# Optimization experiments

Measured on AMD Instinct MI355X. Metric: run time of the kernel, lower is better.

The kernel has to match this reference:

```python
import jax, jax.numpy as jnp
import numpy as np

D = 1024  # input_dim


def setup_inputs() -> dict:
    key = jax.random.key(0)
    ks = jax.random.split(key, 7)
    scale = 1.0 / np.sqrt(D)
    x = jax.random.normal(ks[0], (4, D, 2048), dtype=jnp.float32)
    Wq = jax.random.uniform(ks[1], (D, D), jnp.float32, -scale, scale)
    bq = jax.random.uniform(ks[2], (D,), jnp.float32, -scale, scale)
    Wk = jax.random.uniform(ks[3], (D, D), jnp.float32, -scale, scale)
    bk = jax.random.uniform(ks[4], (D,), jnp.float32, -scale, scale)
    Wv = jax.random.uniform(ks[5], (D, D), jnp.float32, -scale, scale)
    bv = jax.random.uniform(ks[6], (D,), jnp.float32, -scale, scale)
    return {"x": x, "Wq": Wq, "bq": bq, "Wk": Wk, "bk": bk, "Wv": Wv, "bv": bv}


def reference(x, Wq, bq, Wk, bk, Wv, bv):
    # x: [B, D, S] -> [B, S, D]
    xt = jnp.transpose(x, (0, 2, 1))
    # torch nn.Linear: y = x @ W^T + b
    q = jnp.einsum('bsd,ed->bse', xt, Wq) + bq
    k = jnp.einsum('bsd,ed->bse', xt, Wk) + bk
    v = jnp.einsum('bsd,ed->bse', xt, Wv) + bv
    scores = jnp.einsum('bse,bte->bst', q, k) / jnp.sqrt(jnp.float32(D))
    attn = jax.nn.softmax(scores, axis=2)
    out = jnp.einsum('bst,bte->bse', attn, v)  # [B, S, D]
    return out
```

## Files before the change

### kernel.cpp

```cpp
#include <hip/hip_runtime.h>
#include <stdint.h>

typedef unsigned short us16;
typedef unsigned short us8  __attribute__((ext_vector_type(8)));
typedef unsigned short us4v __attribute__((ext_vector_type(4)));
typedef __bf16         bf16x8 __attribute__((ext_vector_type(8)));
typedef float          f32x4  __attribute__((ext_vector_type(4)));

__device__ __forceinline__ us16 f2bf(float f) {
    union { float f; unsigned int u; } c; c.f = f;
    unsigned int u = (c.u + 0x7fffu + ((c.u >> 16) & 1u)) >> 16;
    return (us16)u;
}

__device__ __forceinline__ void async16(const us16* g, us16* l) {
    __builtin_amdgcn_global_load_lds(
        (const __attribute__((address_space(1))) unsigned int*)g,
        (__attribute__((address_space(3))) unsigned int*)l,
        16, 0, 0);
}

template <int EPI, int MI>
__device__ __forceinline__ void gemm_core(
        const us16* __restrict__ A, const us16* __restrict__ B,
        void* __restrict__ C, const float* __restrict__ bias,
        float* __restrict__ L,
        int M, int K, int x, int y, us16* lds) {
    constexpr int BM     = MI * 32;
    constexpr int BOFF   = BM * 64;
    constexpr int BUF    = (BM + 256) * 64;
    constexpr int ACALLS = BM / 64;
    constexpr int PMI    = MI / 4;

    const int tid  = threadIdx.x;
    const int lane = tid & 63, wid = tid >> 6;
    const int l15  = lane & 15, quad = lane >> 4;
    const int wm   = wid >> 2, wn = wid & 3;
    const int m0   = x * BM, n0 = y * 256;

    const int srow = tid >> 3;
    const int sc   = ((tid & 7) ^ (srow & 7)) * 8;
    const us16* Ag = A + (size_t)(m0 + srow) * K + sc;
    const us16* Bg = B + (size_t)(n0 + srow) * K + sc;
    const int sl   = tid * 8;

    f32x4 acc[MI][4] = {};
    const int NT = K >> 6;

#pragma unroll
    for (int c = 0; c < ACALLS; c++) async16(Ag + (size_t)(c * 64) * K, lds + c * 4096 + sl);
#pragma unroll
    for (int c = 0; c < 4; c++)      async16(Bg + (size_t)(c * 64) * K, lds + BOFF + c * 4096 + sl);

    for (int t = 0; t < NT; t++) {
        const us16* cur = lds + (t & 1) * BUF;
        __syncthreads();

        if (t + 1 < NT) {
            us16* nxt = lds + ((t + 1) & 1) * BUF;
            const size_t ko = (size_t)(t + 1) * 64;
#pragma unroll
            for (int c = 0; c < ACALLS; c++) async16(Ag + (size_t)(c * 64) * K + ko, nxt + c * 4096 + sl);
#pragma unroll
            for (int c = 0; c < 4; c++)      async16(Bg + (size_t)(c * 64) * K + ko, nxt + BOFF + c * 4096 + sl);
        }

        bf16x8 bf[4][2];
#pragma unroll
        for (int nj = 0; nj < 4; nj++) {
            const int rb = wn * 64 + nj * 16 + l15;
#pragma unroll
            for (int ks = 0; ks < 2; ks++)
                bf[nj][ks] = *(const bf16x8*)(cur + BOFF + rb * 64 + ((ks * 4 + quad) ^ (rb & 7)) * 8);
        }
        bf16x8 af[2][PMI][2];
#pragma unroll
        for (int i = 0; i < PMI; i++) {
            const int ra = wm * (MI * 16) + i * 16 + l15;
#pragma unroll
            for (int ks = 0; ks < 2; ks++)
                af[0][i][ks] = *(const bf16x8*)(cur + ra * 64 + ((ks * 4 + quad) ^ (ra & 7)) * 8);
        }

#pragma unroll
        for (int p = 0; p < 4; p++) {
            if (p < 3) {
#pragma unroll
                for (int i = 0; i < PMI; i++) {
                    const int ra = wm * (MI * 16) + ((p + 1) * PMI + i) * 16 + l15;
#pragma unroll
                    for (int ks = 0; ks < 2; ks++)
                        af[(p + 1) & 1][i][ks] = *(const bf16x8*)(cur + ra * 64 + ((ks * 4 + quad) ^ (ra & 7)) * 8);
                }
            }
            __builtin_amdgcn_s_setprio(1);
#pragma unroll
            for (int ks = 0; ks < 2; ks++)
#pragma unroll
                for (int i = 0; i < PMI; i++)
#pragma unroll
                    for (int nj = 0; nj < 4; nj++)
                        acc[p * PMI + i][nj] = __builtin_amdgcn_mfma_f32_16x16x32_bf16(
                            af[p & 1][i][ks], bf[nj][ks], acc[p * PMI + i][nj], 0, 0, 0);
            __builtin_amdgcn_s_setprio(0);
        }
    }

    if (EPI == 2) {
        const float scale = 0.03125f;
        float rs[4] = {0.f, 0.f, 0.f, 0.f};
#pragma unroll
        for (int i = 0; i < MI; i++) {
            const int mb = m0 + wm * (MI * 16) + i * 16 + quad * 4;
#pragma unroll
            for (int j = 0; j < 4; j++) {
                const int n = n0 + wn * 64 + j * 16 + l15;
                f32x4 v = acc[i][j];
                const float e0 = __expf(v[0] * scale), e1 = __expf(v[1] * scale);
                const float e2 = __expf(v[2] * scale), e3 = __expf(v[3] * scale);
                rs[j] += (e0 + e1) + (e2 + e3);
                us4v st = { f2bf(e0), f2bf(e1), f2bf(e2), f2bf(e3) };
                *(us4v*)((us16*)C + (size_t)n * M + mb) = st;
            }
        }
#pragma unroll
        for (int j = 0; j < 4; j++) {
            rs[j] += __shfl_xor(rs[j], 16, 64);
            rs[j] += __shfl_xor(rs[j], 32, 64);
        }
        if (quad == 0) {
#pragma unroll
            for (int j = 0; j < 4; j++)
                atomicAdd(&L[n0 + wn * 64 + j * 16 + l15], rs[j]);
        }
        return;
    }

#pragma unroll
    for (int i = 0; i < MI; i++) {
        const int mb = m0 + wm * (MI * 16) + i * 16 + quad * 4;
        float b0 = 0.f, b1 = 0.f, b2 = 0.f, b3 = 0.f;
        if (EPI == 0) {
            float4 bv4 = *(const float4*)(bias + mb);
            b0 = bv4.x; b1 = bv4.y; b2 = bv4.z; b3 = bv4.w;
        }
#pragma unroll
        for (int j = 0; j < 4; j++) {
            const int n = n0 + wn * 64 + j * 16 + l15;
            f32x4 v = acc[i][j];
            if (EPI == 3) {
                const float inv = 1.0f / L[n];
                float4 st;
                st.x = v[0] * inv; st.y = v[1] * inv;
                st.z = v[2] * inv; st.w = v[3] * inv;
                *(float4*)((float*)C + (size_t)n * M + mb) = st;
            } else {
                const float bn = (EPI == 1) ? bias[n] : 0.0f;
                us4v st = { f2bf(v[0] + b0 + bn), f2bf(v[1] + b1 + bn),
                            f2bf(v[2] + b2 + bn), f2bf(v[3] + b3 + bn) };
                *(us4v*)((us16*)C + (size_t)n * M + mb) = st;
            }
        }
    }
}

__device__ __forceinline__ void strip_xy(int lin, int gy, int& x, int& y) {
    const int within = lin & (4 * gy - 1);
    x = (lin / (4 * gy)) * 4 + (within & 3);
    y = within >> 2;
}

__global__ __launch_bounds__(256)
void prep(const float* __restrict__ x, us16* __restrict__ xt,
          const float* __restrict__ wq, const float* __restrict__ wk,
          const float* __restrict__ wv, us16* __restrict__ wb) {
    __shared__ us16 tile[64 * 65];
    const int id = blockIdx.x;
    const int t = threadIdx.x;
    if (id < 2048) {
        const int s0 = (id & 31) * 64, d0 = ((id >> 5) & 15) * 64, b = id >> 9;
        const float* xp = x + ((size_t)b * 1024 + d0) * 2048 + s0;
        const int r = t >> 4, c4 = t & 15;
#pragma unroll
        for (int i = 0; i < 4; i++) {
            float4 v = *(const float4*)(xp + (size_t)(r + 16 * i) * 2048 + c4 * 4);
            const int d = r + 16 * i;
            tile[(c4 * 4 + 0) * 65 + d] = f2bf(v.x);
            tile[(c4 * 4 + 1) * 65 + d] = f2bf(v.y);
            tile[(c4 * 4 + 2) * 65 + d] = f2bf(v.z);
            tile[(c4 * 4 + 3) * 65 + d] = f2bf(v.w);
        }
        __syncthreads();
        us16* op = xt + ((size_t)b * 2048 + s0) * 1024 + d0;
#pragma unroll
        for (int i = 0; i < 2; i++) {
            const int u = t + 256 * i;
            const int s = u >> 3, c8 = u & 7;
            us8 o;
#pragma unroll
            for (int j = 0; j < 8; j++) o[j] = tile[s * 65 + c8 * 8 + j];
            *(us8*)(op + (size_t)s * 1024 + c8 * 8) = o;
        }
    } else {
        const int cid = id - 2048;
        const int mb = cid >> 10;
        const float* src = (mb == 0) ? wq : (mb == 1) ? wk : wv;
        const size_t off = ((size_t)(cid & 1023) * 256 + t) * 4;
        float4 v = *(const float4*)(src + off);
        us4v o = { f2bf(v.x), f2bf(v.y), f2bf(v.z), f2bf(v.w) };
        *(us4v*)(wb + (size_t)mb * 1048576 + off) = o;
    }
}

__global__ __launch_bounds__(512)
void qkv(const us16* __restrict__ Wb, const us16* __restrict__ XT,
         us16* __restrict__ Qb, us16* __restrict__ Kb, us16* __restrict__ VT,
         const float* __restrict__ bq, const float* __restrict__ bk,
         const float* __restrict__ bv) {
    __shared__ __align__(16) us16 lds[65536];
    const int id = blockIdx.x;
    const long long sXT = 2097152;
    if (id < 256) {
        const int z = id >> 5, zz = z & 3;
        const bool isK = z >= 4;
        int x, y; strip_xy(id & 31, 8, x, y);
        const us16* A = Wb + (isK ? 1048576 : 0);
        const us16* B = XT + (size_t)zz * sXT;
        us16* C = (isK ? Kb : Qb) + (size_t)zz * sXT;
        gemm_core<0, 8>(A, B, (void*)C, isK ? bk : bq, nullptr, 1024, 1024, x, y, lds);
    } else {
        const int id2 = id - 256;
        const int z = id2 >> 6;
        int x, y; strip_xy(id2 & 63, 4, x, y);
        gemm_core<1, 4>(XT + (size_t)z * sXT, Wb + 2097152,
                        (void*)(VT + (size_t)z * sXT), bv, nullptr,
                        2048, 1024, x, y, lds);
    }
}

__global__ __launch_bounds__(512)
void scores_k(const us16* __restrict__ Kb, const us16* __restrict__ Qb,
              us16* __restrict__ Sb, float* __restrict__ L) {
    __shared__ __align__(16) us16 lds[65536];
    const long long sXT = 2097152, sSS = 4194304;
    const int z = blockIdx.z;
    int x, y; strip_xy(blockIdx.x + 8 * blockIdx.y, 8, x, y);
    gemm_core<2, 8>(Kb + (size_t)z * sXT, Qb + (size_t)z * sXT,
                    (void*)(Sb + (size_t)z * sSS), nullptr, L + z * 2048,
                    2048, 1024, x, y, lds);
}

__global__ __launch_bounds__(512)
void out_k(const us16* __restrict__ VT, const us16* __restrict__ Sb,
           float* __restrict__ L, float* __restrict__ out) {
    __shared__ __align__(16) us16 lds[49152];
    const long long sXT = 2097152, sSS = 4194304;
    const int z = blockIdx.z;
    int x, y; strip_xy(blockIdx.x + 8 * blockIdx.y, 8, x, y);
    gemm_core<3, 4>(VT + (size_t)z * sXT, Sb + (size_t)z * sSS,
                    (void*)(out + (size_t)z * sXT), nullptr, L + z * 2048,
                    1024, 2048, x, y, lds);
}

extern "C" void kernel_launch(void* const* d_in, const int* in_sizes, int n_in,
                              void* d_out, int out_size, void* d_ws, size_t ws_size,
                              hipStream_t stream) {
    const float* x  = (const float*)d_in[0];
    const float* Wq = (const float*)d_in[1];
    const float* bq = (const float*)d_in[2];
    const float* Wk = (const float*)d_in[3];
    const float* bk = (const float*)d_in[4];
    const float* Wv = (const float*)d_in[5];
    const float* bv = (const float*)d_in[6];
    float* out = (float*)d_out;
    char* ws = (char*)d_ws;

    const size_t SZ = 16777216;
    us16* Qb = (us16*)(ws);
    us16* Kb = (us16*)(ws + SZ);
    us16* VT = (us16*)(ws + 2 * SZ);
    us16* XT = (us16*)(ws + 3 * SZ);
    us16* Wb = (us16*)(ws + 4 * SZ);
    us16* Sb = (us16*)(ws + 3 * SZ);
    float* Lb = (float*)(ws + 5 * SZ);

    hipMemsetAsync(Lb, 0, 4 * 2048 * sizeof(float), stream);
    prep<<<dim3(5120, 1, 1), dim3(256, 1, 1), 0, stream>>>(x, XT, Wq, Wk, Wv, Wb);
    qkv<<<dim3(512, 1, 1), dim3(512, 1, 1), 0, stream>>>(Wb, XT, Qb, Kb, VT, bq, bk, bv);
    scores_k<<<dim3(8, 8, 4), dim3(512, 1, 1), 0, stream>>>(Kb, Qb, Sb, Lb);
    out_k<<<dim3(8, 8, 4), dim3(512, 1, 1), 0, stream>>>(VT, Sb, Lb, out);
}
```

Measured before the change: 222.7 us.

## Software-pipeline LDS fragment loads across k-tiles with split last-phase MFMAs

The GEMM main loop is restructured so the first B and A fragments of the next k-tile are read from LDS while the last phase's MFMAs of the current tile are still issuing. The final phase is split into two halves of the N columns, with the B fragment reloads interleaved between them after a vmcnt wait and barrier. The aim is to hide LDS read latency at the tile boundary so the MFMA pipe is not left idle. In exchange there is an extra barrier per iteration, higher register pressure, and a more fragile ordering between the async global-to-LDS loads and the reads that follow them.

```diff
diff --git a/kernel.cpp b/kernel.cpp
--- a/kernel.cpp
+++ b/kernel.cpp
@@ -51,47 +51,46 @@
     for (int c = 0; c < ACALLS; c++) async16(Ag + (size_t)(c * 64) * K, lds + c * 4096 + sl);
 #pragma unroll
     for (int c = 0; c < 4; c++)      async16(Bg + (size_t)(c * 64) * K, lds + BOFF + c * 4096 + sl);
+    __syncthreads();
+
+    bf16x8 bf[4][2];
+    bf16x8 af[2][PMI][2];
+#pragma unroll
+    for (int nj = 0; nj < 4; nj++) {
+        const int rb = wn * 64 + nj * 16 + l15;
+#pragma unroll
+        for (int ks = 0; ks < 2; ks++)
+            bf[nj][ks] = *(const bf16x8*)(lds + BOFF + rb * 64 + ((ks * 4 + quad) ^ (rb & 7)) * 8);
+    }
+#pragma unroll
+    for (int i = 0; i < PMI; i++) {
+        const int ra = wm * (MI * 16) + i * 16 + l15;
+#pragma unroll
+        for (int ks = 0; ks < 2; ks++)
+            af[0][i][ks] = *(const bf16x8*)(lds + ra * 64 + ((ks * 4 + quad) ^ (ra & 7)) * 8);
+    }
 
     for (int t = 0; t < NT; t++) {
         const us16* cur = lds + (t & 1) * BUF;
-        __syncthreads();
+        const us16* nxt = lds + ((t + 1) & 1) * BUF;
 
         if (t + 1 < NT) {
-            us16* nxt = lds + ((t + 1) & 1) * BUF;
+            us16* nb = lds + ((t + 1) & 1) * BUF;
             const size_t ko = (size_t)(t + 1) * 64;
 #pragma unroll
-            for (int c = 0; c < ACALLS; c++) async16(Ag + (size_t)(c * 64) * K + ko, nxt + c * 4096 + sl);
-#pragma unroll
-            for (int c = 0; c < 4; c++)      async16(Bg + (size_t)(c * 64) * K + ko, nxt + BOFF + c * 4096 + sl);
-        }
-
-        bf16x8 bf[4][2];
-#pragma unroll
-        for (int nj = 0; nj < 4; nj++) {
-            const int rb = wn * 64 + nj * 16 + l15;
-#pragma unroll
-            for (int ks = 0; ks < 2; ks++)
-                bf[nj][ks] = *(const bf16x8*)(cur + BOFF + rb * 64 + ((ks * 4 + quad) ^ (rb & 7)) * 8);
-        }
-        bf16x8 af[2][PMI][2];
-#pragma unroll
-        for (int i = 0; i < PMI; i++) {
-            const int ra = wm * (MI * 16) + i * 16 + l15;
-#pragma unroll
-            for (int ks = 0; ks < 2; ks++)
-                af[0][i][ks] = *(const bf16x8*)(cur + ra * 64 + ((ks * 4 + quad) ^ (ra & 7)) * 8);
-        }
-
-#pragma unroll
-        for (int p = 0; p < 4; p++) {
-            if (p < 3) {
-#pragma unroll
-                for (int i = 0; i < PMI; i++) {
-                    const int ra = wm * (MI * 16) + ((p + 1) * PMI + i) * 16 + l15;
-#pragma unroll
-                    for (int ks = 0; ks < 2; ks++)
-                        af[(p + 1) & 1][i][ks] = *(const bf16x8*)(cur + ra * 64 + ((ks * 4 + quad) ^ (ra & 7)) * 8);
-                }
+            for (int c = 0; c < ACALLS; c++) async16(Ag + (size_t)(c * 64) * K + ko, nb + c * 4096 + sl);
+#pragma unroll
+            for (int c = 0; c < 4; c++)      async16(Bg + (size_t)(c * 64) * K + ko, nb + BOFF + c * 4096 + sl);
+        }
+
+#pragma unroll
+        for (int p = 0; p < 3; p++) {
+#pragma unroll
+            for (int i = 0; i < PMI; i++) {
+                const int ra = wm * (MI * 16) + ((p + 1) * PMI + i) * 16 + l15;
+#pragma unroll
+                for (int ks = 0; ks < 2; ks++)
+                    af[(p + 1) & 1][i][ks] = *(const bf16x8*)(cur + ra * 64 + ((ks * 4 + quad) ^ (ra & 7)) * 8);
             }
             __builtin_amdgcn_s_setprio(1);
 #pragma unroll
@@ -104,6 +103,65 @@
                             af[p & 1][i][ks], bf[nj][ks], acc[p * PMI + i][nj], 0, 0, 0);
             __builtin_amdgcn_s_setprio(0);
         }
+
+        if (t + 1 < NT) {
+            asm volatile("s_waitcnt vmcnt(0)" ::: "memory");
+            __builtin_amdgcn_s_barrier();
+            __builtin_amdgcn_sched_barrier(0);
+            __builtin_amdgcn_s_setprio(1);
+#pragma unroll
+            for (int ks = 0; ks < 2; ks++)
+#pragma unroll
+                for (int i = 0; i < PMI; i++)
+#pragma unroll
+                    for (int nj = 0; nj < 2; nj++)
+                        acc[3 * PMI + i][nj] = __builtin_amdgcn_mfma_f32_16x16x32_bf16(
+                            af[1][i][ks], bf[nj][ks], acc[3 * PMI + i][nj], 0, 0, 0);
+            __builtin_amdgcn_s_setprio(0);
+#pragma unroll
+            for (int nj = 0; nj < 2; nj++) {
+                const int rb = wn * 64 + nj * 16 + l15;
+#pragma unroll
+                for (int ks = 0; ks < 2; ks++)
+                    bf[nj][ks] = *(const bf16x8*)(nxt + BOFF + rb * 64 + ((ks * 4 + quad) ^ (rb & 7)) * 8);
+            }
+            __builtin_amdgcn_s_setprio(1);
+#pragma unroll
+            for (int ks = 0; ks < 2; ks++)
+#pragma unroll
+                for (int i = 0; i < PMI; i++)
+#pragma unroll
+                    for (int nj = 2; nj < 4; nj++)
+                        acc[3 * PMI + i][nj] = __builtin_amdgcn_mfma_f32_16x16x32_bf16(
+                            af[1][i][ks], bf[nj][ks], acc[3 * PMI + i][nj], 0, 0, 0);
+            __builtin_amdgcn_s_setprio(0);
+#pragma unroll
+            for (int nj = 2; nj < 4; nj++) {
+                const int rb = wn * 64 + nj * 16 + l15;
+#pragma unroll
+                for (int ks = 0; ks < 2; ks++)
+                    bf[nj][ks] = *(const bf16x8*)(nxt + BOFF + rb * 64 + ((ks * 4 + quad) ^ (rb & 7)) * 8);
+            }
+#pragma unroll
+            for (int i = 0; i < PMI; i++) {
+                const int ra = wm * (MI * 16) + i * 16 + l15;
+#pragma unroll
+                for (int ks = 0; ks < 2; ks++)
+                    af[0][i][ks] = *(const bf16x8*)(nxt + ra * 64 + ((ks * 4 + quad) ^ (ra & 7)) * 8);
+            }
+        } else {
+            __builtin_amdgcn_s_setprio(1);
+#pragma unroll
+            for (int ks = 0; ks < 2; ks++)
+#pragma unroll
+                for (int i = 0; i < PMI; i++)
+#pragma unroll
+                    for (int nj = 0; nj < 4; nj++)
+                        acc[3 * PMI + i][nj] = __builtin_amdgcn_mfma_f32_16x16x32_bf16(
+                            af[1][i][ks], bf[nj][ks], acc[3 * PMI + i][nj], 0, 0, 0);
+            __builtin_amdgcn_s_setprio(0);
+        }
+        __syncthreads();
     }
 
     if (EPI == 2) {
```

Measured after the change: 236.4 us. +6.2%, slower.

## Switch GEMM core to 32x32x16 MFMA tiles and fold L-buffer memset into prep

Applied to the files above, without the earlier changes.

The shared GEMM core now uses 32x32x16 bf16 MFMA instructions with 16-wide accumulators in place of 16x16x32 ones, and the LDS fragment loads and all epilogues (bias, exp/row-sum, normalize) are remapped to the 32x32 output layout. Block tile sizes stay the same. The larger MFMA shape cuts the LDS fragment reads per FLOP and the instruction count. Separately, the hipMemsetAsync that zeroed the softmax denominator buffer is replaced by four extra blocks in the prep kernel, removing one launch. The new epilogue indexing changes store patterns and must match the 32x32 accumulator layout to stay correct.

```diff
diff --git a/kernel.cpp b/kernel.cpp
--- a/kernel.cpp
+++ b/kernel.cpp
@@ -5,7 +5,7 @@
 typedef unsigned short us8  __attribute__((ext_vector_type(8)));
 typedef unsigned short us4v __attribute__((ext_vector_type(4)));
 typedef __bf16         bf16x8 __attribute__((ext_vector_type(8)));
-typedef float          f32x4  __attribute__((ext_vector_type(4)));
+typedef float          f32x16 __attribute__((ext_vector_type(16)));
 
 __device__ __forceinline__ us16 f2bf(float f) {
     union { float f; unsigned int u; } c; c.f = f;
@@ -20,21 +20,20 @@
         16, 0, 0);
 }
 
-template <int EPI, int MI>
+template <int EPI, int MF>
 __device__ __forceinline__ void gemm_core(
         const us16* __restrict__ A, const us16* __restrict__ B,
         void* __restrict__ C, const float* __restrict__ bias,
         float* __restrict__ L,
         int M, int K, int x, int y, us16* lds) {
-    constexpr int BM     = MI * 32;
+    constexpr int BM     = MF * 64;
     constexpr int BOFF   = BM * 64;
     constexpr int BUF    = (BM + 256) * 64;
-    constexpr int ACALLS = BM / 64;
-    constexpr int PMI    = MI / 4;
+    constexpr int ACALLS = MF;
 
     const int tid  = threadIdx.x;
     const int lane = tid & 63, wid = tid >> 6;
-    const int l15  = lane & 15, quad = lane >> 4;
+    const int l31  = lane & 31, half = lane >> 5;
     const int wm   = wid >> 2, wn = wid & 3;
     const int m0   = x * BM, n0 = y * 256;
 
@@ -44,7 +43,7 @@
     const us16* Bg = B + (size_t)(n0 + srow) * K + sc;
     const int sl   = tid * 8;
 
-    f32x4 acc[MI][4] = {};
+    f32x16 acc[MF][2] = {};
     const int NT = K >> 6;
 
 #pragma unroll
@@ -65,100 +64,102 @@
             for (int c = 0; c < 4; c++)      async16(Bg + (size_t)(c * 64) * K + ko, nxt + BOFF + c * 4096 + sl);
         }
 
-        bf16x8 bf[4][2];
-#pragma unroll
-        for (int nj = 0; nj < 4; nj++) {
-            const int rb = wn * 64 + nj * 16 + l15;
-#pragma unroll
-            for (int ks = 0; ks < 2; ks++)
-                bf[nj][ks] = *(const bf16x8*)(cur + BOFF + rb * 64 + ((ks * 4 + quad) ^ (rb & 7)) * 8);
-        }
-        bf16x8 af[2][PMI][2];
-#pragma unroll
-        for (int i = 0; i < PMI; i++) {
-            const int ra = wm * (MI * 16) + i * 16 + l15;
-#pragma unroll
-            for (int ks = 0; ks < 2; ks++)
-                af[0][i][ks] = *(const bf16x8*)(cur + ra * 64 + ((ks * 4 + quad) ^ (ra & 7)) * 8);
-        }
-
-#pragma unroll
-        for (int p = 0; p < 4; p++) {
-            if (p < 3) {
-#pragma unroll
-                for (int i = 0; i < PMI; i++) {
-                    const int ra = wm * (MI * 16) + ((p + 1) * PMI + i) * 16 + l15;
-#pragma unroll
-                    for (int ks = 0; ks < 2; ks++)
-                        af[(p + 1) & 1][i][ks] = *(const bf16x8*)(cur + ra * 64 + ((ks * 4 + quad) ^ (ra & 7)) * 8);
+        bf16x8 bf[2][4];
+#pragma unroll
+        for (int nf = 0; nf < 2; nf++) {
+            const int rb = wn * 64 + nf * 32 + l31;
+#pragma unroll
+            for (int ks = 0; ks < 4; ks++)
+                bf[nf][ks] = *(const bf16x8*)(cur + BOFF + rb * 64 + ((ks * 2 + half) ^ (rb & 7)) * 8);
+        }
+        bf16x8 af[2][4];
+        {
+            const int ra = wm * (MF * 32) + l31;
+#pragma unroll
+            for (int ks = 0; ks < 4; ks++)
+                af[0][ks] = *(const bf16x8*)(cur + ra * 64 + ((ks * 2 + half) ^ (ra & 7)) * 8);
+        }
+
+#pragma unroll
+        for (int p = 0; p < MF; p++) {
+            if (p + 1 < MF) {
+                const int ra = wm * (MF * 32) + (p + 1) * 32 + l31;
+#pragma unroll
+                for (int ks = 0; ks < 4; ks++)
+                    af[(p + 1) & 1][ks] = *(const bf16x8*)(cur + ra * 64 + ((ks * 2 + half) ^ (ra & 7)) * 8);
+            }
+            __builtin_amdgcn_s_setprio(1);
+#pragma unroll
+            for (int ks = 0; ks < 4; ks++)
+#pragma unroll
+                for (int nf = 0; nf < 2; nf++)
+                    acc[p][nf] = __builtin_amdgcn_mfma_f32_32x32x16_bf16(
+                        af[p & 1][ks], bf[nf][ks], acc[p][nf], 0, 0, 0);
+            __builtin_amdgcn_s_setprio(0);
+        }
+    }
+
+    if (EPI == 2) {
+        const float scale = 0.03125f;
+        float rs[2] = {0.f, 0.f};
+#pragma unroll
+        for (int mf = 0; mf < MF; mf++) {
+#pragma unroll
+            for (int nf = 0; nf < 2; nf++) {
+                const int n = n0 + wn * 64 + nf * 32 + l31;
+                const int mbase = m0 + wm * (MF * 32) + mf * 32 + 4 * half;
+                f32x16 v = acc[mf][nf];
+#pragma unroll
+                for (int g = 0; g < 4; g++) {
+                    const float e0 = __expf(v[4 * g + 0] * scale);
+                    const float e1 = __expf(v[4 * g + 1] * scale);
+                    const float e2 = __expf(v[4 * g + 2] * scale);
+                    const float e3 = __expf(v[4 * g + 3] * scale);
+                    rs[nf] += (e0 + e1) + (e2 + e3);
+                    us4v st = { f2bf(e0), f2bf(e1), f2bf(e2), f2bf(e3) };
+                    *(us4v*)((us16*)C + (size_t)n * M + mbase + 8 * g) = st;
                 }
             }
-            __builtin_amdgcn_s_setprio(1);
-#pragma unroll
-            for (int ks = 0; ks < 2; ks++)
-#pragma unroll
-                for (int i = 0; i < PMI; i++)
-#pragma unroll
-                    for (int nj = 0; nj < 4; nj++)
-                        acc[p * PMI + i][nj] = __builtin_amdgcn_mfma_f32_16x16x32_bf16(
-                            af[p & 1][i][ks], bf[nj][ks], acc[p * PMI + i][nj], 0, 0, 0);
-            __builtin_amdgcn_s_setprio(0);
-        }
-    }
-
-    if (EPI == 2) {
-        const float scale = 0.03125f;
-        float rs[4] = {0.f, 0.f, 0.f, 0.f};
-#pragma unroll
-        for (int i = 0; i < MI; i++) {
-            const int mb = m0 + wm * (MI * 16) + i * 16 + quad * 4;
-#pragma unroll
-            for (int j = 0; j < 4; j++) {
-                const int n = n0 + wn * 64 + j * 16 + l15;
-                f32x4 v = acc[i][j];
-                const float e0 = __expf(v[0] * scale), e1 = __expf(v[1] * scale);
-                const float e2 = __expf(v[2] * scale), e3 = __expf(v[3] * scale);
-                rs[j] += (e0 + e1) + (e2 + e3);
-                us4v st = { f2bf(e0), f2bf(e1), f2bf(e2), f2bf(e3) };
-                *(us4v*)((us16*)C + (size_t)n * M + mb) = st;
-            }
-        }
-#pragma unroll
-        for (int j = 0; j < 4; j++) {
-            rs[j] += __shfl_xor(rs[j], 16, 64);
-            rs[j] += __shfl_xor(rs[j], 32, 64);
-        }
-        if (quad == 0) {
-#pragma unroll
-            for (int j = 0; j < 4; j++)
-                atomicAdd(&L[n0 + wn * 64 + j * 16 + l15], rs[j]);
+        }
+#pragma unroll
+        for (int nf = 0; nf < 2; nf++) rs[nf] += __shfl_xor(rs[nf], 32, 64);
+        if (half == 0) {
+#pragma unroll
+            for (int nf = 0; nf < 2; nf++)
+                atomicAdd(&L[n0 + wn * 64 + nf * 32 + l31], rs[nf]);
         }
         return;
     }
 
 #pragma unroll
-    for (int i = 0; i < MI; i++) {
-        const int mb = m0 + wm * (MI * 16) + i * 16 + quad * 4;
-        float b0 = 0.f, b1 = 0.f, b2 = 0.f, b3 = 0.f;
-        if (EPI == 0) {
-            float4 bv4 = *(const float4*)(bias + mb);
-            b0 = bv4.x; b1 = bv4.y; b2 = bv4.z; b3 = bv4.w;
-        }
-#pragma unroll
-        for (int j = 0; j < 4; j++) {
-            const int n = n0 + wn * 64 + j * 16 + l15;
-            f32x4 v = acc[i][j];
+    for (int mf = 0; mf < MF; mf++) {
+#pragma unroll
+        for (int nf = 0; nf < 2; nf++) {
+            const int n = n0 + wn * 64 + nf * 32 + l31;
+            const int mbase = m0 + wm * (MF * 32) + mf * 32 + 4 * half;
+            f32x16 v = acc[mf][nf];
             if (EPI == 3) {
                 const float inv = 1.0f / L[n];
-                float4 st;
-                st.x = v[0] * inv; st.y = v[1] * inv;
-                st.z = v[2] * inv; st.w = v[3] * inv;
-                *(float4*)((float*)C + (size_t)n * M + mb) = st;
+#pragma unroll
+                for (int g = 0; g < 4; g++) {
+                    float4 st;
+                    st.x = v[4 * g + 0] * inv; st.y = v[4 * g + 1] * inv;
+                    st.z = v[4 * g + 2] * inv; st.w = v[4 * g + 3] * inv;
+                    *(float4*)((float*)C + (size_t)n * M + mbase + 8 * g) = st;
+                }
             } else {
                 const float bn = (EPI == 1) ? bias[n] : 0.0f;
-                us4v st = { f2bf(v[0] + b0 + bn), f2bf(v[1] + b1 + bn),
-                            f2bf(v[2] + b2 + bn), f2bf(v[3] + b3 + bn) };
-                *(us4v*)((us16*)C + (size_t)n * M + mb) = st;
+#pragma unroll
+                for (int g = 0; g < 4; g++) {
+                    float b0 = bn, b1 = bn, b2 = bn, b3 = bn;
+                    if (EPI == 0) {
+                        float4 bv4 = *(const float4*)(bias + mbase + 8 * g);
+                        b0 = bv4.x; b1 = bv4.y; b2 = bv4.z; b3 = bv4.w;
+                    }
+                    us4v st = { f2bf(v[4 * g + 0] + b0), f2bf(v[4 * g + 1] + b1),
+                                f2bf(v[4 * g + 2] + b2), f2bf(v[4 * g + 3] + b3) };
+                    *(us4v*)((us16*)C + (size_t)n * M + mbase + 8 * g) = st;
+                }
             }
         }
     }
@@ -173,7 +174,8 @@
 __global__ __launch_bounds__(256)
 void prep(const float* __restrict__ x, us16* __restrict__ xt,
           const float* __restrict__ wq, const float* __restrict__ wk,
-          const float* __restrict__ wv, us16* __restrict__ wb) {
+          const float* __restrict__ wv, us16* __restrict__ wb,
+          float* __restrict__ Lb) {
     __shared__ us16 tile[64 * 65];
     const int id = blockIdx.x;
     const int t = threadIdx.x;
@@ -201,7 +203,7 @@
             for (int j = 0; j < 8; j++) o[j] = tile[s * 65 + c8 * 8 + j];
             *(us8*)(op + (size_t)s * 1024 + c8 * 8) = o;
         }
-    } else {
+    } else if (id < 5120) {
         const int cid = id - 2048;
         const int mb = cid >> 10;
         const float* src = (mb == 0) ? wq : (mb == 1) ? wk : wv;
@@ -209,6 +211,11 @@
         float4 v = *(const float4*)(src + off);
         us4v o = { f2bf(v.x), f2bf(v.y), f2bf(v.z), f2bf(v.w) };
         *(us4v*)(wb + (size_t)mb * 1048576 + off) = o;
+    } else {
+        float4 z = { 0.f, 0.f, 0.f, 0.f };
+        float* p = Lb + (size_t)(id - 5120) * 2048 + t * 8;
+        *(float4*)(p) = z;
+        *(float4*)(p + 4) = z;
     }
 }
 
@@ -227,12 +234,12 @@
         const us16* A = Wb + (isK ? 1048576 : 0);
         const us16* B = XT + (size_t)zz * sXT;
         us16* C = (isK ? Kb : Qb) + (size_t)zz * sXT;
-        gemm_core<0, 8>(A, B, (void*)C, isK ? bk : bq, nullptr, 1024, 1024, x, y, lds);
+        gemm_core<0, 4>(A, B, (void*)C, isK ? bk : bq, nullptr, 1024, 1024, x, y, lds);
     } else {
         const int id2 = id - 256;
         const int z = id2 >> 6;
         int x, y; strip_xy(id2 & 63, 4, x, y);
-        gemm_core<1, 4>(XT + (size_t)z * sXT, Wb + 2097152,
+        gemm_core<1, 2>(XT + (size_t)z * sXT, Wb + 2097152,
                         (void*)(VT + (size_t)z * sXT), bv, nullptr,
                         2048, 1024, x, y, lds);
     }
@@ -245,7 +252,7 @@
     const long long sXT = 2097152, sSS = 4194304;
     const int z = blockIdx.z;
     int x, y; strip_xy(blockIdx.x + 8 * blockIdx.y, 8, x, y);
-    gemm_core<2, 8>(Kb + (size_t)z * sXT, Qb + (size_t)z * sXT,
+    gemm_core<2, 4>(Kb + (size_t)z * sXT, Qb + (size_t)z * sXT,
                     (void*)(Sb + (size_t)z * sSS), nullptr, L + z * 2048,
                     2048, 1024, x, y, lds);
 }
@@ -257,7 +264,7 @@
     const long long sXT = 2097152, sSS = 4194304;
     const int z = blockIdx.z;
     int x, y; strip_xy(blockIdx.x + 8 * blockIdx.y, 8, x, y);
-    gemm_core<3, 4>(VT + (size_t)z * sXT, Sb + (size_t)z * sSS,
+    gemm_core<3, 2>(VT + (size_t)z * sXT, Sb + (size_t)z * sSS,
                     (void*)(out + (size_t)z * sXT), nullptr, L + z * 2048,
                     1024, 2048, x, y, lds);
 }
@@ -284,8 +291,7 @@
     us16* Sb = (us16*)(ws + 3 * SZ);
     float* Lb = (float*)(ws + 5 * SZ);
 
-    hipMemsetAsync(Lb, 0, 4 * 2048 * sizeof(float), stream);
-    prep<<<dim3(5120, 1, 1), dim3(256, 1, 1), 0, stream>>>(x, XT, Wq, Wk, Wv, Wb);
+    prep<<<dim3(5124, 1, 1), dim3(256, 1, 1), 0, stream>>>(x, XT, Wq, Wk, Wv, Wb, Lb);
     qkv<<<dim3(512, 1, 1), dim3(512, 1, 1), 0, stream>>>(Wb, XT, Qb, Kb, VT, bq, bk, bv);
     scores_k<<<dim3(8, 8, 4), dim3(512, 1, 1), 0, stream>>>(Kb, Qb, Sb, Lb);
     out_k<<<dim3(8, 8, 4), dim3(512, 1, 1), 0, stream>>>(VT, Sb, Lb, out);
```

Measured after the change: 233.1 us. 4.7% more time.

## Single-buffer LDS in QKV GEMM and fold L zeroing into prep

Applied to the files above, without the earlier changes.

Adds a single-buffered mode to the shared GEMM core and uses it for the QKV projection kernel, halving its LDS allocation so more workgroups can be resident per CU. In that mode each K-step loads, synchronizes and then computes, giving up the overlap of global loads with MFMA work in exchange for occupancy. Separately, the memset of the softmax normalizer buffer is removed and done by four extra blocks in the prep kernel, saving one launch.

```diff
diff --git a/kernel.cpp b/kernel.cpp
--- a/kernel.cpp
+++ b/kernel.cpp
@@ -20,7 +20,7 @@
         16, 0, 0);
 }
 
-template <int EPI, int MI>
+template <int EPI, int MI, bool SB>
 __device__ __forceinline__ void gemm_core(
         const us16* __restrict__ A, const us16* __restrict__ B,
         void* __restrict__ C, const float* __restrict__ bias,
@@ -47,22 +47,35 @@
     f32x4 acc[MI][4] = {};
     const int NT = K >> 6;
 
-#pragma unroll
-    for (int c = 0; c < ACALLS; c++) async16(Ag + (size_t)(c * 64) * K, lds + c * 4096 + sl);
-#pragma unroll
-    for (int c = 0; c < 4; c++)      async16(Bg + (size_t)(c * 64) * K, lds + BOFF + c * 4096 + sl);
+    if (!SB) {
+#pragma unroll
+        for (int c = 0; c < ACALLS; c++) async16(Ag + (size_t)(c * 64) * K, lds + c * 4096 + sl);
+#pragma unroll
+        for (int c = 0; c < 4; c++)      async16(Bg + (size_t)(c * 64) * K, lds + BOFF + c * 4096 + sl);
+    }
 
     for (int t = 0; t < NT; t++) {
-        const us16* cur = lds + (t & 1) * BUF;
-        __syncthreads();
-
-        if (t + 1 < NT) {
-            us16* nxt = lds + ((t + 1) & 1) * BUF;
-            const size_t ko = (size_t)(t + 1) * 64;
-#pragma unroll
-            for (int c = 0; c < ACALLS; c++) async16(Ag + (size_t)(c * 64) * K + ko, nxt + c * 4096 + sl);
-#pragma unroll
-            for (int c = 0; c < 4; c++)      async16(Bg + (size_t)(c * 64) * K + ko, nxt + BOFF + c * 4096 + sl);
+        const us16* cur;
+        if (SB) {
+            if (t) __syncthreads();
+            const size_t ko = (size_t)t * 64;
+#pragma unroll
+            for (int c = 0; c < ACALLS; c++) async16(Ag + (size_t)(c * 64) * K + ko, lds + c * 4096 + sl);
+#pragma unroll
+            for (int c = 0; c < 4; c++)      async16(Bg + (size_t)(c * 64) * K + ko, lds + BOFF + c * 4096 + sl);
+            __syncthreads();
+            cur = lds;
+        } else {
+            cur = lds + (t & 1) * BUF;
+            __syncthreads();
+            if (t + 1 < NT) {
+                us16* nxt = lds + ((t + 1) & 1) * BUF;
+                const size_t ko = (size_t)(t + 1) * 64;
+#pragma unroll
+                for (int c = 0; c < ACALLS; c++) async16(Ag + (size_t)(c * 64) * K + ko, nxt + c * 4096 + sl);
+#pragma unroll
+                for (int c = 0; c < 4; c++)      async16(Bg + (size_t)(c * 64) * K + ko, nxt + BOFF + c * 4096 + sl);
+            }
         }
 
         bf16x8 bf[4][2];
@@ -173,7 +186,8 @@
 __global__ __launch_bounds__(256)
 void prep(const float* __restrict__ x, us16* __restrict__ xt,
           const float* __restrict__ wq, const float* __restrict__ wk,
-          const float* __restrict__ wv, us16* __restrict__ wb) {
+          const float* __restrict__ wv, us16* __restrict__ wb,
+          float* __restrict__ Lb) {
     __shared__ us16 tile[64 * 65];
     const int id = blockIdx.x;
     const int t = threadIdx.x;
@@ -201,7 +215,7 @@
             for (int j = 0; j < 8; j++) o[j] = tile[s * 65 + c8 * 8 + j];
             *(us8*)(op + (size_t)s * 1024 + c8 * 8) = o;
         }
-    } else {
+    } else if (id < 5120) {
         const int cid = id - 2048;
         const int mb = cid >> 10;
         const float* src = (mb == 0) ? wq : (mb == 1) ? wk : wv;
@@ -209,6 +223,11 @@
         float4 v = *(const float4*)(src + off);
         us4v o = { f2bf(v.x), f2bf(v.y), f2bf(v.z), f2bf(v.w) };
         *(us4v*)(wb + (size_t)mb * 1048576 + off) = o;
+    } else {
+        float4 z = { 0.f, 0.f, 0.f, 0.f };
+        float* p = Lb + (size_t)(id - 5120) * 2048 + t * 8;
+        *(float4*)(p) = z;
+        *(float4*)(p + 4) = z;
     }
 }
 
@@ -217,7 +236,7 @@
          us16* __restrict__ Qb, us16* __restrict__ Kb, us16* __restrict__ VT,
          const float* __restrict__ bq, const float* __restrict__ bk,
          const float* __restrict__ bv) {
-    __shared__ __align__(16) us16 lds[65536];
+    __shared__ __align__(16) us16 lds[32768];
     const int id = blockIdx.x;
     const long long sXT = 2097152;
     if (id < 256) {
@@ -227,14 +246,14 @@
         const us16* A = Wb + (isK ? 1048576 : 0);
         const us16* B = XT + (size_t)zz * sXT;
         us16* C = (isK ? Kb : Qb) + (size_t)zz * sXT;
-        gemm_core<0, 8>(A, B, (void*)C, isK ? bk : bq, nullptr, 1024, 1024, x, y, lds);
+        gemm_core<0, 8, true>(A, B, (void*)C, isK ? bk : bq, nullptr, 1024, 1024, x, y, lds);
     } else {
         const int id2 = id - 256;
         const int z = id2 >> 6;
         int x, y; strip_xy(id2 & 63, 4, x, y);
-        gemm_core<1, 4>(XT + (size_t)z * sXT, Wb + 2097152,
-                        (void*)(VT + (size_t)z * sXT), bv, nullptr,
-                        2048, 1024, x, y, lds);
+        gemm_core<1, 4, true>(XT + (size_t)z * sXT, Wb + 2097152,
+                              (void*)(VT + (size_t)z * sXT), bv, nullptr,
+                              2048, 1024, x, y, lds);
     }
 }
 
@@ -245,9 +264,9 @@
     const long long sXT = 2097152, sSS = 4194304;
     const int z = blockIdx.z;
     int x, y; strip_xy(blockIdx.x + 8 * blockIdx.y, 8, x, y);
-    gemm_core<2, 8>(Kb + (size_t)z * sXT, Qb + (size_t)z * sXT,
-                    (void*)(Sb + (size_t)z * sSS), nullptr, L + z * 2048,
-                    2048, 1024, x, y, lds);
+    gemm_core<2, 8, false>(Kb + (size_t)z * sXT, Qb + (size_t)z * sXT,
+                           (void*)(Sb + (size_t)z * sSS), nullptr, L + z * 2048,
+                           2048, 1024, x, y, lds);
 }
 
 __global__ __launch_bounds__(512)
@@ -257,9 +276,9 @@
     const long long sXT = 2097152, sSS = 4194304;
     const int z = blockIdx.z;
     int x, y; strip_xy(blockIdx.x + 8 * blockIdx.y, 8, x, y);
-    gemm_core<3, 4>(VT + (size_t)z * sXT, Sb + (size_t)z * sSS,
-                    (void*)(out + (size_t)z * sXT), nullptr, L + z * 2048,
-                    1024, 2048, x, y, lds);
+    gemm_core<3, 4, false>(VT + (size_t)z * sXT, Sb + (size_t)z * sSS,
+                           (void*)(out + (size_t)z * sXT), nullptr, L + z * 2048,
+                           1024, 2048, x, y, lds);
 }
 
 extern "C" void kernel_launch(void* const* d_in, const int* in_sizes, int n_in,
@@ -284,8 +303,7 @@
     us16* Sb = (us16*)(ws + 3 * SZ);
     float* Lb = (float*)(ws + 5 * SZ);
 
-    hipMemsetAsync(Lb, 0, 4 * 2048 * sizeof(float), stream);
-    prep<<<dim3(5120, 1, 1), dim3(256, 1, 1), 0, stream>>>(x, XT, Wq, Wk, Wv, Wb);
+    prep<<<dim3(5124, 1, 1), dim3(256, 1, 1), 0, stream>>>(x, XT, Wq, Wk, Wv, Wb, Lb);
     qkv<<<dim3(512, 1, 1), dim3(512, 1, 1), 0, stream>>>(Wb, XT, Qb, Kb, VT, bq, bk, bv);
     scores_k<<<dim3(8, 8, 4), dim3(512, 1, 1), 0, stream>>>(Kb, Qb, Sb, Lb);
     out_k<<<dim3(8, 8, 4), dim3(512, 1, 1), 0, stream>>>(VT, Sb, Lb, out);
```

Measured after the change: 240.9 us. +8.2%, slower.
